# Kernel optimization log

Hardware: AMD Instinct MI355X
Metric: run time of the kernel (lower is better)

Reference implementation:

```python
import jax, jax.numpy as jnp
import numpy as np

N = 1_048_576   # nodes
E = 8_388_608   # edges
G = 32_768      # graphs
D = 9           # node embedding dim (hardcoded emb_dim=9 in source)
H = 2 * D       # GIN MLP hidden
L = 3           # num_layers
ATOM_V, BOND_V = 119, 6
BN_EPS = 1e-5


def setup_inputs() -> dict:
    key = jax.random.key(0)
    ks = jax.random.split(key, 12)
    f = lambda i, shape: jax.random.normal(ks[i], shape, jnp.float32) * 0.1
    return {
        'atom_emb': f(0, (9, ATOM_V, D)),
        'bond_emb': f(1, (L, 3, BOND_V, D)),
        'eps_gin': jnp.zeros((L,), jnp.float32),
        'W1': f(2, (L, D, H)), 'b1': jnp.zeros((L, H)),
        'bn1_g': jnp.ones((L, H)), 'bn1_b': jnp.zeros((L, H)),
        'W2': f(3, (L, H, D)), 'b2': jnp.zeros((L, D)),
        'bno_g': jnp.ones((L, D)), 'bno_b': jnp.zeros((L, D)),
        'vnW1': f(4, (L - 1, D, H)), 'vnb1': jnp.zeros((L - 1, H)),
        'vnbn1_g': jnp.ones((L - 1, H)), 'vnbn1_b': jnp.zeros((L - 1, H)),
        'vnW2': f(5, (L - 1, H, D)), 'vnb2': jnp.zeros((L - 1, D)),
        'vnbn2_g': jnp.ones((L - 1, D)), 'vnbn2_b': jnp.zeros((L - 1, D)),
        'x': jax.random.randint(ks[6], (N, 9), 0, 2),
        'edge_index': jax.random.randint(ks[7], (2, E), 0, N),
        'edge_attr': jax.random.randint(ks[8], (E, 3), 0, 2),
        'batch': jnp.sort(jax.random.randint(ks[9], (N,), 0, G)),
        'num_graphs': G,
    }


def _bn(h, g, b):
    # BatchNorm1d in training mode: batch mean / biased variance
    m = h.mean(axis=0)
    v = h.var(axis=0)
    return (h - m) * jax.lax.rsqrt(v + BN_EPS) * g + b


def reference(atom_emb, bond_emb, eps_gin, W1, b1, bn1_g, bn1_b, W2, b2,
              bno_g, bno_b, vnW1, vnb1, vnbn1_g, vnbn1_b, vnW2, vnb2,
              vnbn2_g, vnbn2_b, x, edge_index, edge_attr, batch, num_graphs):
    n_nodes = x.shape[0]
    src, dst = edge_index[0], edge_index[1]
    # AtomEncoder: sum of per-field embeddings -> [N, D]
    h = atom_emb[jnp.arange(atom_emb.shape[0])[None, :], x].sum(axis=1)
    vn = jnp.zeros((num_graphs, h.shape[1]), h.dtype)  # virtualnode emb init 0
    num_layers = W1.shape[0]
    for l in range(num_layers):
        h_in = h + vn[batch]                              # broadcast VN to nodes
        # BondEncoder for this layer -> [E, D]
        e = bond_emb[l][jnp.arange(3)[None, :], edge_attr].sum(axis=1)
        # GIN message: relu(x_j + e), sum-aggregate at target
        msg = jax.nn.relu(h_in[src] + e)
        aggr = jax.ops.segment_sum(msg, dst, num_segments=n_nodes)
        z = (1.0 + eps_gin[l]) * h_in + aggr
        z = jax.nn.relu(_bn(z @ W1[l] + b1[l], bn1_g[l], bn1_b[l])) @ W2[l] + b2[l]
        z = _bn(z, bno_g[l], bno_b[l])
        if l < num_layers - 1:
            z = jax.nn.relu(z)
        h_new = z + h_in                                   # residual=True
        if l < num_layers - 1:
            vn_tmp = jax.ops.segment_sum(h_in, batch, num_segments=num_graphs) + vn
            t = jax.nn.relu(_bn(vn_tmp @ vnW1[l] + vnb1[l], vnbn1_g[l], vnbn1_b[l]))
            t = jax.nn.relu(_bn(t @ vnW2[l] + vnb2[l], vnbn2_g[l], vnbn2_b[l]))
            vn = vn + t                                    # VN residual
        h = h_new
    pooled = jax.ops.segment_sum(h, batch, num_segments=num_graphs)  # global_add_pool
    return jnp.sum(pooled, axis=0, keepdims=True)          # [1, D]
```

## Files before the change

### kernel.cpp

```cpp
#include <hip/hip_runtime.h>
#include <hip/hip_fp8.h>

#define NN 1048576
#define NE 8388608
#define NG 32768
#define DD 9
#define SB 12
#define HH 18
#define BN_EPS 1e-5f

#define NPB 512
#define NB  2048
#define NGRP 64
#define P1B 512
#define P3MAX 5120
#define P3KEYS 4096

#define NSUM1 0
#define NSQ1  18
#define NSUM2 36
#define NSQ2  45
#define OUTS  54
#define VBASE 4096
#define VSUM1 (VBASE+0)
#define VSQ1  (VBASE+18)
#define VSUM2 (VBASE+36)
#define VSQ2  (VBASE+45)
#define STATS_FLOATS 4224

typedef float fv4 __attribute__((ext_vector_type(4)));

__device__ __forceinline__ float waveReduce(float v) {
#pragma unroll
  for (int off = 32; off > 0; off >>= 1) v += __shfl_down(v, off, 64);
  return v;
}
__device__ __forceinline__ unsigned f8enc(float f) {
  __hip_fp8_e4m3 v(f);
  return (unsigned)v.__x;
}
__device__ __forceinline__ float f8dec(unsigned b) {
  __hip_fp8_e4m3 v;
  v.__x = (__hip_fp8_storage_t)b;
  return (float)v;
}


__global__ void __launch_bounds__(1024)
k_counthist(const int* __restrict__ ei, int* __restrict__ cnt_pad,
            int* __restrict__ blkcnt) {
  __shared__ int hist[NB];
  int tid = threadIdx.x;
  for (int i = tid; i < NB; i += 1024) hist[i] = 0;
  __syncthreads();
  const int CH = NE / P1B;
  int base = blockIdx.x * CH;
  for (int i = tid; i < CH; i += 1024)
    atomicAdd(&hist[ei[NE + base + i] >> 9], 1);
  __syncthreads();
  for (int i = tid; i < NB; i += 1024)
    if (hist[i]) atomicAdd(&cnt_pad[i * 16], hist[i]);
  if (tid < NGRP) {
    int s = 0;
#pragma unroll
    for (int k = 0; k < 32; ++k) s += hist[tid * 32 + k];
    blkcnt[tid * P1B + blockIdx.x] = s;
  }
}

__global__ void k_scan(const int* __restrict__ cnt_pad, int* __restrict__ bucket_base,
                       int* __restrict__ bucket_cursor) {
  __shared__ int tsum[256];
  int tid = threadIdx.x;
  int c[8];
  int run = 0;
#pragma unroll
  for (int k = 0; k < 8; ++k) { c[k] = cnt_pad[(tid * 8 + k) * 16]; run += c[k]; }
  tsum[tid] = run;
  __syncthreads();
  for (int off = 1; off < 256; off <<= 1) {
    int v = (tid >= off) ? tsum[tid - off] : 0;
    __syncthreads();
    tsum[tid] += v;
    __syncthreads();
  }
  int excl = tsum[tid] - run;
#pragma unroll
  for (int k = 0; k < 8; ++k) {
    bucket_base[tid * 8 + k] = excl;
    bucket_cursor[tid * 8 + k] = excl;
    excl += c[k];
  }
  if (tid == 255) bucket_base[NB] = tsum[255];
}

__global__ void k_scanG(int* __restrict__ blkcnt, const int* __restrict__ bucket_base) {
  __shared__ int tsum[256];
  int tid = threadIdx.x;
  int g = blockIdx.x;
  int c0 = blkcnt[g * P1B + 2 * tid], c1 = blkcnt[g * P1B + 2 * tid + 1];
  int run = c0 + c1;
  tsum[tid] = run;
  __syncthreads();
  for (int off = 1; off < 256; off <<= 1) {
    int v = (tid >= off) ? tsum[tid - off] : 0;
    __syncthreads();
    tsum[tid] += v;
    __syncthreads();
  }
  int excl = tsum[tid] - run + bucket_base[g << 5];
  blkcnt[g * P1B + 2 * tid] = excl;
  blkcnt[g * P1B + 2 * tid + 1] = excl + c0;
}

__global__ void __launch_bounds__(1024)
k_p1(const int* __restrict__ ei, const int* __restrict__ ea,
     const int* __restrict__ blkcnt, uint2* __restrict__ coarse) {
  __shared__ int lcnt[NGRP];
  __shared__ int lbase[NGRP];
  int tid = threadIdx.x;
  if (tid < NGRP) { lcnt[tid] = 0; lbase[tid] = blkcnt[tid * P1B + blockIdx.x]; }
  __syncthreads();
  const int CH = NE / P1B;
  int base = blockIdx.x * CH;
  for (int k = 0; k < CH / 1024; ++k) {
    int e = base + k * 1024 + tid;
    int s = ei[e];
    int d = ei[NE + e];
    unsigned at = (unsigned)((ea[(size_t)e * 3 + 0] & 1) |
                             ((ea[(size_t)e * 3 + 1] & 1) << 1) |
                             ((ea[(size_t)e * 3 + 2] & 1) << 2));
    int g = d >> 14;
    int pos = atomicAdd(&lcnt[g], 1);
    coarse[lbase[g] + pos] = make_uint2((unsigned)s | (at << 20), (unsigned)d);
  }
}

#define P2K 48
#define P2SUB 32
__global__ void __launch_bounds__(256)
k_p2(const uint2* __restrict__ coarse, const int* __restrict__ bucket_base,
     int* __restrict__ bucket_cursor, unsigned* __restrict__ binned) {
  __shared__ unsigned stage[32 * P2K];
  __shared__ int scnt[32], gbase[32];
  int tid = threadIdx.x;
  int g = blockIdx.x >> 5;
  int sub = blockIdx.x & 31;
  int s0 = bucket_base[g << 5];
  int s1 = bucket_base[(g + 1) << 5];
  int len = s1 - s0;
  int chunk = (len + P2SUB - 1) >> 5;
  int my0 = s0 + sub * chunk;
  int my1 = min(my0 + chunk, s1);
  if (tid < 32) scnt[tid] = 0;
  __syncthreads();
  for (int b0 = my0; b0 < my1; b0 += 1024) {
#pragma unroll
    for (int k = 0; k < 4; ++k) {
      int i = b0 + k * 256 + tid;
      if (i < my1) {
        uint2 rec = coarse[i];
        unsigned s = rec.x & 0xFFFFFu;
        unsigned at = rec.x >> 20;
        unsigned d = rec.y;
        int bt = (int)((d >> 9) & 31u);
        unsigned o = s | ((d & 511u) << 20) | (at << 29);
        int pos = atomicAdd(&scnt[bt], 1);
        if (pos < P2K) stage[bt * P2K + pos] = o;
        else binned[atomicAdd(&bucket_cursor[(g << 5) | bt], 1)] = o;
      }
    }
    __syncthreads();
    {
      int bt = tid >> 3, j = tid & 7;
      int cnt = min(scnt[bt], P2K);
      if (j == 0) gbase[bt] = cnt ? atomicAdd(&bucket_cursor[(g << 5) | bt], cnt) : 0;
      __syncthreads();
      for (int i = j; i < cnt; i += 8) binned[gbase[bt] + i] = stage[bt * P2K + i];
    }
    __syncthreads();
    if (tid < 32) scnt[tid] = 0;
    __syncthreads();
  }
}

__global__ void __launch_bounds__(256)
k_p3(unsigned* __restrict__ binned, const int* __restrict__ bucket_base,
     int* __restrict__ row_ptr) {
  __shared__ int cnt[P3KEYS];
  __shared__ int tsum[256];
  __shared__ unsigned stage[P3MAX];
  int tid = threadIdx.x;
  int b = blockIdx.x;
  int s0 = bucket_base[b], s1 = bucket_base[b + 1];
  int len = s1 - s0;
  for (int i = tid; i < P3KEYS; i += 256) cnt[i] = 0;
  __syncthreads();
  for (int i = tid; i < len; i += 256) {
    unsigned rec = binned[s0 + i];
    int key = (int)((((rec >> 20) & 511u) << 3) | ((rec & 0xFFFFFu) >> 17));
    atomicAdd(&cnt[key], 1);
  }
  __syncthreads();
  int c[16];
  int run = 0;
#pragma unroll
  for (int k = 0; k < 16; ++k) { c[k] = cnt[tid * 16 + k]; run += c[k]; }
  tsum[tid] = run;
  __syncthreads();
  for (int off = 1; off < 256; off <<= 1) {
    int v = (tid >= off) ? tsum[tid - off] : 0;
    __syncthreads();
    tsum[tid] += v;
    __syncthreads();
  }
  int excl = tsum[tid] - run;
  int sum8 = 0;
#pragma unroll
  for (int k = 0; k < 8; ++k) sum8 += c[k];
  row_ptr[b * NPB + 2 * tid] = s0 + excl;
  row_ptr[b * NPB + 2 * tid + 1] = s0 + excl + sum8;
  if (b == NB - 1 && tid == 255) row_ptr[NN] = s0 + excl + run;
  int e = excl;
#pragma unroll
  for (int k = 0; k < 16; ++k) { cnt[tid * 16 + k] = e; e += c[k]; }
  __syncthreads();
  for (int i = tid; i < len; i += 256) {
    unsigned rec = binned[s0 + i];
    int key = (int)((((rec >> 20) & 511u) << 3) | ((rec & 0xFFFFFu) >> 17));
    int pos = atomicAdd(&cnt[key], 1);
    stage[pos] = (rec & 0xFFFFFu) | ((rec >> 29) << 20);
  }
  __syncthreads();
  for (int i = tid; i < len; i += 256) binned[s0 + i] = stage[i];
}


__device__ __forceinline__ void writeMirror(uint2* __restrict__ hmA,
                                            unsigned char* __restrict__ hmB,
                                            size_t n, const float* hv) {
  uint2 q;
  q.x = f8enc(hv[0]) | (f8enc(hv[1]) << 8) | (f8enc(hv[2]) << 16) | (f8enc(hv[3]) << 24);
  q.y = f8enc(hv[4]) | (f8enc(hv[5]) << 8) | (f8enc(hv[6]) << 16) | (f8enc(hv[7]) << 24);
  hmA[n] = q;
  hmB[n] = (unsigned char)f8enc(hv[8]);
}

__global__ void k_atom(const float* __restrict__ atom_emb, const int* __restrict__ x,
                       const int* __restrict__ batch, float* __restrict__ h,
                       uint2* __restrict__ hmA, unsigned char* __restrict__ hmB,
                       float* __restrict__ vnsum) {
  int n = blockIdx.x * 256 + threadIdx.x;
  int xi[9];
#pragma unroll
  for (int f = 0; f < 9; ++f) xi[f] = x[(size_t)n * 9 + f];
  float acc[DD] = {0.f,0.f,0.f,0.f,0.f,0.f,0.f,0.f,0.f};
#pragma unroll
  for (int f = 0; f < 9; ++f) {
    const float* row = atom_emb + ((size_t)f * 119 + xi[f]) * DD;
#pragma unroll
    for (int d = 0; d < DD; ++d) acc[d] += row[d];
  }
  float* o = h + (size_t)n * SB;
  ((float4*)o)[0] = make_float4(acc[0], acc[1], acc[2], acc[3]);
  ((float4*)o)[1] = make_float4(acc[4], acc[5], acc[6], acc[7]);
  o[8] = acc[8];
  writeMirror(hmA, hmB, (size_t)n, acc);
  int g = batch[n];
  int lane = threadIdx.x & 63;
  float s[DD];
#pragma unroll
  for (int d = 0; d < DD; ++d) s[d] = acc[d];
#pragma unroll
  for (int st = 1; st < 64; st <<= 1) {
    int gu = __shfl_up(g, st, 64);
    bool ok = (lane >= st) && (gu == g);
#pragma unroll
    for (int d = 0; d < DD; ++d) {
      float vu = __shfl_up(s[d], st, 64);
      if (ok) s[d] += vu;
    }
  }
  int gn = __shfl_down(g, 1, 64);
  if ((lane == 63) || (gn != g)) {
#pragma unroll
    for (int d = 0; d < DD; ++d) atomicAdd(&vnsum[(size_t)g * DD + d], s[d]);
  }
}

__device__ __forceinline__ void edgeDecodeAcc(unsigned r, uint2 q, unsigned db,
                                              const float* __restrict__ comb,
                                              float* __restrict__ acc) {
  const float* cb = comb + (r >> 20) * DD;
  float hv[DD] = {f8dec(q.x & 255u), f8dec((q.x >> 8) & 255u),
                  f8dec((q.x >> 16) & 255u), f8dec(q.x >> 24),
                  f8dec(q.y & 255u), f8dec((q.y >> 8) & 255u),
                  f8dec((q.y >> 16) & 255u), f8dec(q.y >> 24),
                  f8dec(db)};
#pragma unroll
  for (int d = 0; d < DD; ++d) {
    float m = hv[d] + cb[d];
    m = m > 0.f ? m : 0.f;
    acc[d] += m;
  }
}

__device__ __forceinline__ void accumNode(const unsigned* __restrict__ binned,
                                          int e0, int e1,
                                          const uint2* __restrict__ hmA,
                                          const unsigned char* __restrict__ hmB,
                                          const float* __restrict__ comb,
                                          float* __restrict__ acc) {
  int i = e0;
  for (; i + 4 <= e1; i += 4) {
    unsigned r0 = binned[i], r1 = binned[i + 1], r2 = binned[i + 2], r3 = binned[i + 3];
    uint2 q0 = hmA[r0 & 0xFFFFFu];
    uint2 q1 = hmA[r1 & 0xFFFFFu];
    uint2 q2 = hmA[r2 & 0xFFFFFu];
    uint2 q3 = hmA[r3 & 0xFFFFFu];
    unsigned char d0 = hmB[r0 & 0xFFFFFu];
    unsigned char d1 = hmB[r1 & 0xFFFFFu];
    unsigned char d2 = hmB[r2 & 0xFFFFFu];
    unsigned char d3 = hmB[r3 & 0xFFFFFu];
    edgeDecodeAcc(r0, q0, d0, comb, acc);
    edgeDecodeAcc(r1, q1, d1, comb, acc);
    edgeDecodeAcc(r2, q2, d2, comb, acc);
    edgeDecodeAcc(r3, q3, d3, comb, acc);
  }
  for (; i < e1; ++i) {
    unsigned r = binned[i];
    uint2 q = hmA[r & 0xFFFFFu];
    unsigned char db = hmB[r & 0xFFFFFu];
    edgeDecodeAcc(r, q, db, comb, acc);
  }
}

__global__ void __launch_bounds__(256, 8)
k_edgeA(const float* __restrict__ hbuf, const uint2* __restrict__ hmA,
        const unsigned char* __restrict__ hmB, const unsigned* __restrict__ binned,
        const int* __restrict__ row_ptr, const float* __restrict__ bond,
        const float* __restrict__ W1l, const float* __restrict__ b1l,
        const float* __restrict__ epsp, float* __restrict__ X,
        float* __restrict__ stats) {
  __shared__ float comb[8 * DD];
  __shared__ float sW1[DD * HH], sb1[HH], ssum[HH], ssq[HH];
  int tid = threadIdx.x;
  for (int i = tid; i < DD * HH; i += 256) sW1[i] = W1l[i];
  if (tid < 8 * DD) {
    int c = tid / DD, d = tid % DD;
    comb[tid] = bond[(0 * 6 + (c & 1)) * DD + d] +
                bond[(1 * 6 + ((c >> 1) & 1)) * DD + d] +
                bond[(2 * 6 + ((c >> 2) & 1)) * DD + d];
  }
  if (tid < HH) { sb1[tid] = b1l[tid]; ssum[tid] = 0.f; ssq[tid] = 0.f; }
  __syncthreads();

  int b = blockIdx.x;
  int nA = b * NPB + tid;
  int nB = nA + 256;
  int ea0 = row_ptr[nA], ea1 = row_ptr[nA + 1];
  int eb0 = row_ptr[nB], eb1 = row_ptr[nB + 1];
  float acc0[DD] = {0.f,0.f,0.f,0.f,0.f,0.f,0.f,0.f,0.f};
  float acc1[DD] = {0.f,0.f,0.f,0.f,0.f,0.f,0.f,0.f,0.f};
  accumNode(binned, ea0, ea1, hmA, hmB, comb, acc0);
  accumNode(binned, eb0, eb1, hmA, hmB, comb, acc1);

  float eps1 = 1.0f + epsp[0];
  float z0[DD], z1[DD];
  {
    const float* hr = hbuf + (size_t)nA * SB;
    float4 HA = ((const float4*)hr)[0], HB = ((const float4*)hr)[1];
    float h8 = hr[8];
    float hi[DD] = {HA.x, HA.y, HA.z, HA.w, HB.x, HB.y, HB.z, HB.w, h8};
#pragma unroll
    for (int d = 0; d < DD; ++d) z0[d] = eps1 * hi[d] + acc0[d];
    float* xo = X + (size_t)nA * SB;
    fv4 v0 = {z0[0], z0[1], z0[2], z0[3]};
    fv4 v1 = {z0[4], z0[5], z0[6], z0[7]};
    __builtin_nontemporal_store(v0, (fv4*)xo);
    __builtin_nontemporal_store(v1, (fv4*)(xo + 4));
    __builtin_nontemporal_store(z0[8], xo + 8);
  }
  {
    const float* hr = hbuf + (size_t)nB * SB;
    float4 HA = ((const float4*)hr)[0], HB = ((const float4*)hr)[1];
    float h8 = hr[8];
    float hi[DD] = {HA.x, HA.y, HA.z, HA.w, HB.x, HB.y, HB.z, HB.w, h8};
#pragma unroll
    for (int d = 0; d < DD; ++d) z1[d] = eps1 * hi[d] + acc1[d];
    float* xo = X + (size_t)nB * SB;
    fv4 v0 = {z1[0], z1[1], z1[2], z1[3]};
    fv4 v1 = {z1[4], z1[5], z1[6], z1[7]};
    __builtin_nontemporal_store(v0, (fv4*)xo);
    __builtin_nontemporal_store(v1, (fv4*)(xo + 4));
    __builtin_nontemporal_store(z1[8], xo + 8);
  }
  int lane0 = ((tid & 63) == 0);
#pragma unroll
  for (int j = 0; j < HH; ++j) {
    float a0 = sb1[j], a1 = sb1[j];
#pragma unroll
    for (int d = 0; d < DD; ++d) {
      a0 += z0[d] * sW1[d * HH + j];
      a1 += z1[d] * sW1[d * HH + j];
    }
    float rs = waveReduce(a0 + a1);
    float rq = waveReduce(a0 * a0 + a1 * a1);
    if (lane0) { atomicAdd(&ssum[j], rs); atomicAdd(&ssq[j], rq); }
  }
  __syncthreads();
  int copy = (b & 63) * 64;
  if (tid < HH) {
    atomicAdd(&stats[copy + NSUM1 + tid], ssum[tid]);
    atomicAdd(&stats[copy + NSQ1 + tid], ssq[tid]);
  }
}

__global__ void __launch_bounds__(256)
k_partB(float* __restrict__ X, const float* __restrict__ W1l, const float* __restrict__ b1l,
        const float* __restrict__ g1, const float* __restrict__ be1,
        const float* __restrict__ W2l, const float* __restrict__ b2l,
        float* __restrict__ stats) {
  __shared__ float sW1[DD * HH], sW2[HH * DD], sb1[HH], sb2[DD];
  __shared__ float sc1[HH], sh1[HH], ssum[DD], ssq[DD];
  int tid = threadIdx.x;
  for (int i = tid; i < DD * HH; i += 256) sW1[i] = W1l[i];
  for (int i = tid; i < HH * DD; i += 256) sW2[i] = W2l[i];
  if (tid < HH) {
    float s = 0.f, q = 0.f;
#pragma unroll
    for (int c = 0; c < 64; ++c) {
      s += stats[c * 64 + NSUM1 + tid];
      q += stats[c * 64 + NSQ1 + tid];
    }
    float mean = s * (1.0f / NN);
    float var = q * (1.0f / NN) - mean * mean;
    float sc = g1[tid] * rsqrtf(var + BN_EPS);
    sc1[tid] = sc;
    sh1[tid] = be1[tid] - mean * sc;
    sb1[tid] = b1l[tid];
  }
  if (tid < DD) { sb2[tid] = b2l[tid]; ssum[tid] = 0.f; ssq[tid] = 0.f; }
  __syncthreads();
  size_t n = (size_t)blockIdx.x * 256 + tid;
  float* xr = X + n * SB;
  fv4 XA = __builtin_nontemporal_load((const fv4*)xr);
  fv4 XB = __builtin_nontemporal_load((const fv4*)(xr + 4));
  float x8 = __builtin_nontemporal_load(xr + 8);
  float z[DD] = {XA.x, XA.y, XA.z, XA.w, XB.x, XB.y, XB.z, XB.w, x8};
  float t[HH];
#pragma unroll
  for (int j = 0; j < HH; ++j) {
    float a = sb1[j];
#pragma unroll
    for (int d = 0; d < DD; ++d) a += z[d] * sW1[d * HH + j];
    a = a * sc1[j] + sh1[j];
    t[j] = a > 0.f ? a : 0.f;
  }
  float z2[DD];
  int lane0 = ((tid & 63) == 0);
#pragma unroll
  for (int d = 0; d < DD; ++d) {
    float a = sb2[d];
#pragma unroll
    for (int j = 0; j < HH; ++j) a += t[j] * sW2[j * DD + d];
    z2[d] = a;
    float rs = waveReduce(a);
    float rq = waveReduce(a * a);
    if (lane0) { atomicAdd(&ssum[d], rs); atomicAdd(&ssq[d], rq); }
  }
  fv4 v0 = {z2[0], z2[1], z2[2], z2[3]};
  fv4 v1 = {z2[4], z2[5], z2[6], z2[7]};
  __builtin_nontemporal_store(v0, (fv4*)xr);
  __builtin_nontemporal_store(v1, (fv4*)(xr + 4));
  __builtin_nontemporal_store(z2[8], xr + 8);
  __syncthreads();
  int copy = ((int)blockIdx.x & 63) * 64;
  if (tid < DD) {
    atomicAdd(&stats[copy + NSUM2 + tid], ssum[tid]);
    atomicAdd(&stats[copy + NSQ2 + tid], ssq[tid]);
  }
}

__global__ void __launch_bounds__(256)
k_partC(const float* __restrict__ X, float* __restrict__ hbuf,
        uint2* __restrict__ hmA, unsigned char* __restrict__ hmB,
        float* __restrict__ stats, const float* __restrict__ g2,
        const float* __restrict__ be2, const int* __restrict__ batch,
        const float* __restrict__ vn_next, float* __restrict__ vnsum_out,
        int do_relu) {
  __shared__ float sc[DD], sh[DD], ssum[DD];
  int tid = threadIdx.x;
  if (tid < DD) {
    float s = 0.f, q = 0.f;
#pragma unroll
    for (int c = 0; c < 64; ++c) {
      s += stats[c * 64 + NSUM2 + tid];
      q += stats[c * 64 + NSQ2 + tid];
    }
    float mean = s * (1.0f / NN);
    float var = q * (1.0f / NN) - mean * mean;
    float sg = g2[tid] * rsqrtf(var + BN_EPS);
    sc[tid] = sg;
    sh[tid] = be2[tid] - mean * sg;
    ssum[tid] = 0.f;
  }
  __syncthreads();
  size_t n = (size_t)blockIdx.x * 256 + tid;
  const float* xr = X + n * SB;
  fv4 XA = __builtin_nontemporal_load((const fv4*)xr);
  fv4 XB = __builtin_nontemporal_load((const fv4*)(xr + 4));
  float x8 = __builtin_nontemporal_load(xr + 8);
  float zv[DD] = {XA.x, XA.y, XA.z, XA.w, XB.x, XB.y, XB.z, XB.w, x8};
  float* hr = hbuf + n * SB;
  float4 HA = ((float4*)hr)[0], HB = ((float4*)hr)[1];
  float h8 = hr[8];
  float hi[DD] = {HA.x, HA.y, HA.z, HA.w, HB.x, HB.y, HB.z, HB.w, h8};
  float hv[DD];
#pragma unroll
  for (int d = 0; d < DD; ++d) {
    float z = zv[d] * sc[d] + sh[d];
    if (do_relu) z = z > 0.f ? z : 0.f;
    hv[d] = z + hi[d];
  }
  if (vn_next != nullptr) {
    int g = batch[n];
#pragma unroll
    for (int d = 0; d < DD; ++d) hv[d] += vn_next[(size_t)g * DD + d];
    ((float4*)hr)[0] = make_float4(hv[0], hv[1], hv[2], hv[3]);
    ((float4*)hr)[1] = make_float4(hv[4], hv[5], hv[6], hv[7]);
    hr[8] = hv[8];
    writeMirror(hmA, hmB, n, hv);
    if (vnsum_out != nullptr) {
      int lane = tid & 63;
      float s[DD];
#pragma unroll
      for (int d = 0; d < DD; ++d) s[d] = hv[d];
#pragma unroll
      for (int st = 1; st < 64; st <<= 1) {
        int gu = __shfl_up(g, st, 64);
        bool ok = (lane >= st) && (gu == g);
#pragma unroll
        for (int d = 0; d < DD; ++d) {
          float vu = __shfl_up(s[d], st, 64);
          if (ok) s[d] += vu;
        }
      }
      int gn = __shfl_down(g, 1, 64);
      if ((lane == 63) || (gn != g)) {
#pragma unroll
        for (int d = 0; d < DD; ++d) atomicAdd(&vnsum_out[(size_t)g * DD + d], s[d]);
      }
    }
  } else {
    int lane0 = ((tid & 63) == 0);
#pragma unroll
    for (int d = 0; d < DD; ++d) {
      float r = waveReduce(hv[d]);
      if (lane0) atomicAdd(&ssum[d], r);
    }
    __syncthreads();
    int copy = ((int)blockIdx.x & 63) * 64;
    if (tid < DD) atomicAdd(&stats[copy + OUTS + tid], ssum[tid]);
  }
}

__global__ void k_out(const float* __restrict__ stats, float* __restrict__ out) {
  int tid = threadIdx.x;
  if (tid < DD) {
    float s = 0.f;
#pragma unroll
    for (int c = 0; c < 64; ++c) s += stats[c * 64 + OUTS + tid];
    out[tid] = s;
  }
}


__global__ void k_vnA(const float* __restrict__ vnsum, const float* __restrict__ vn,
                      float* __restrict__ vt1, const float* __restrict__ W1l,
                      const float* __restrict__ b1l, float* __restrict__ stats) {
  __shared__ float sW[DD * HH], sb[HH], ssum[HH], ssq[HH];
  int tid = threadIdx.x;
  for (int i = tid; i < DD * HH; i += 256) sW[i] = W1l[i];
  if (tid < HH) { sb[tid] = b1l[tid]; ssum[tid] = 0.f; ssq[tid] = 0.f; }
  __syncthreads();
  size_t g = (size_t)blockIdx.x * 256 + tid;
  float r[DD];
#pragma unroll
  for (int d = 0; d < DD; ++d) r[d] = vnsum[g * DD + d] + vn[g * DD + d];
  int lane0 = ((tid & 63) == 0);
#pragma unroll
  for (int j = 0; j < HH; ++j) {
    float a = sb[j];
#pragma unroll
    for (int d = 0; d < DD; ++d) a += r[d] * sW[d * HH + j];
    vt1[g * HH + j] = a;
    float rs = waveReduce(a);
    float rq = waveReduce(a * a);
    if (lane0) { atomicAdd(&ssum[j], rs); atomicAdd(&ssq[j], rq); }
  }
  __syncthreads();
  if (tid < HH) {
    atomicAdd(&stats[VSUM1 + tid], ssum[tid]);
    atomicAdd(&stats[VSQ1 + tid], ssq[tid]);
  }
}

__global__ void k_vnB(const float* __restrict__ vt1, float* __restrict__ vt2,
                      const float* __restrict__ W2l, const float* __restrict__ b2l,
                      const float* __restrict__ g1, const float* __restrict__ be1,
                      float* __restrict__ stats) {
  __shared__ float sW2[HH * DD], sb2[DD], sc1[HH], sh1[HH], ssum[DD], ssq[DD];
  int tid = threadIdx.x;
  for (int i = tid; i < HH * DD; i += 256) sW2[i] = W2l[i];
  if (tid < HH) {
    float mean = stats[VSUM1 + tid] * (1.0f / NG);
    float var = stats[VSQ1 + tid] * (1.0f / NG) - mean * mean;
    float sc = g1[tid] * rsqrtf(var + BN_EPS);
    sc1[tid] = sc;
    sh1[tid] = be1[tid] - mean * sc;
  }
  if (tid < DD) { sb2[tid] = b2l[tid]; ssum[tid] = 0.f; ssq[tid] = 0.f; }
  __syncthreads();
  size_t g = (size_t)blockIdx.x * 256 + tid;
  float t[HH];
#pragma unroll
  for (int j = 0; j < HH; ++j) {
    float a = vt1[g * HH + j] * sc1[j] + sh1[j];
    t[j] = a > 0.f ? a : 0.f;
  }
  int lane0 = ((tid & 63) == 0);
#pragma unroll
  for (int d = 0; d < DD; ++d) {
    float a = sb2[d];
#pragma unroll
    for (int j = 0; j < HH; ++j) a += t[j] * sW2[j * DD + d];
    vt2[g * DD + d] = a;
    float rs = waveReduce(a);
    float rq = waveReduce(a * a);
    if (lane0) { atomicAdd(&ssum[d], rs); atomicAdd(&ssq[d], rq); }
  }
  __syncthreads();
  if (tid < DD) {
    atomicAdd(&stats[VSUM2 + tid], ssum[tid]);
    atomicAdd(&stats[VSQ2 + tid], ssq[tid]);
  }
}

__global__ void k_vnC(const float* __restrict__ vt2, float* __restrict__ vn,
                      const float* __restrict__ g2, const float* __restrict__ be2,
                      const float* __restrict__ stats) {
  __shared__ float sc[DD], sh[DD];
  int tid = threadIdx.x;
  if (tid < DD) {
    float mean = stats[VSUM2 + tid] * (1.0f / NG);
    float var = stats[VSQ2 + tid] * (1.0f / NG) - mean * mean;
    float s = g2[tid] * rsqrtf(var + BN_EPS);
    sc[tid] = s;
    sh[tid] = be2[tid] - mean * s;
  }
  __syncthreads();
  size_t g = (size_t)blockIdx.x * 256 + tid;
#pragma unroll
  for (int d = 0; d < DD; ++d) {
    float v = vt2[g * DD + d] * sc[d] + sh[d];
    v = v > 0.f ? v : 0.f;
    vn[g * DD + d] += v;
  }
}

extern "C" void kernel_launch(void* const* d_in, const int* in_sizes, int n_in,
                              void* d_out, int out_size, void* d_ws, size_t ws_size,
                              hipStream_t stream) {
  const float* atom_emb = (const float*)d_in[0];
  const float* bond_emb = (const float*)d_in[1];
  const float* eps_gin  = (const float*)d_in[2];
  const float* W1   = (const float*)d_in[3];
  const float* b1   = (const float*)d_in[4];
  const float* bn1_g = (const float*)d_in[5];
  const float* bn1_b = (const float*)d_in[6];
  const float* W2   = (const float*)d_in[7];
  const float* b2   = (const float*)d_in[8];
  const float* bno_g = (const float*)d_in[9];
  const float* bno_b = (const float*)d_in[10];
  const float* vnW1 = (const float*)d_in[11];
  const float* vnb1 = (const float*)d_in[12];
  const float* vnbn1_g = (const float*)d_in[13];
  const float* vnbn1_b = (const float*)d_in[14];
  const float* vnW2 = (const float*)d_in[15];
  const float* vnb2 = (const float*)d_in[16];
  const float* vnbn2_g = (const float*)d_in[17];
  const float* vnbn2_b = (const float*)d_in[18];
  const int* x          = (const int*)d_in[19];
  const int* edge_index = (const int*)d_in[20];
  const int* edge_attr  = (const int*)d_in[21];
  const int* batch      = (const int*)d_in[22];
  float* out = (float*)d_out;

  float* hbuf  = (float*)d_ws;
  float* X     = hbuf + (size_t)NN * SB;
  uint2* hmA   = (uint2*)(X + (size_t)NN * SB);
  unsigned char* hmB = (unsigned char*)(hmA + (size_t)NN);
  unsigned* binned = (unsigned*)(hmB + (size_t)NN);
  float* vn    = (float*)(binned + (size_t)NE);
  float* vnsum = vn + (size_t)NG * DD;
  float* vt2   = vnsum;
  float* vt1   = vnsum + (size_t)NG * DD;
  float* stats = vt1 + (size_t)NG * HH;
  int* bucket_base   = (int*)(stats + STATS_FLOATS);
  int* bucket_cursor = bucket_base + NB + 1;
  int* row_ptr       = bucket_cursor + NB;
  uint2* coarse = (uint2*)d_ws;
  int* cnt_pad  = (int*)((char*)d_ws + (size_t)NE * sizeof(uint2));
  int* blkcnt   = cnt_pad + (size_t)NB * 16;

  (void)hipMemsetAsync(cnt_pad, 0, (size_t)NB * 16 * sizeof(int), stream);
  k_counthist<<<P1B, 1024, 0, stream>>>(edge_index, cnt_pad, blkcnt);
  k_scan<<<1, 256, 0, stream>>>(cnt_pad, bucket_base, bucket_cursor);
  k_scanG<<<NGRP, 256, 0, stream>>>(blkcnt, bucket_base);
  k_p1<<<P1B, 1024, 0, stream>>>(edge_index, edge_attr, blkcnt, coarse);
  k_p2<<<NGRP * P2SUB, 256, 0, stream>>>(coarse, bucket_base, bucket_cursor, binned);
  k_p3<<<NB, 256, 0, stream>>>(binned, bucket_base, row_ptr);

  (void)hipMemsetAsync(vn, 0, (size_t)2 * NG * DD * sizeof(float), stream);
  k_atom<<<NN / 256, 256, 0, stream>>>(atom_emb, x, batch, hbuf, hmA, hmB, vnsum);

  for (int l = 0; l < 3; ++l) {
    int has_vn = (l < 2);
    (void)hipMemsetAsync(stats, 0, STATS_FLOATS * sizeof(float), stream);
    if (has_vn) {
      k_vnA<<<NG / 256, 256, 0, stream>>>(vnsum, vn, vt1, vnW1 + (size_t)l * DD * HH,
                                          vnb1 + (size_t)l * HH, stats);
      k_vnB<<<NG / 256, 256, 0, stream>>>(vt1, vt2, vnW2 + (size_t)l * HH * DD,
                                          vnb2 + (size_t)l * DD,
                                          vnbn1_g + (size_t)l * HH, vnbn1_b + (size_t)l * HH,
                                          stats);
      k_vnC<<<NG / 256, 256, 0, stream>>>(vt2, vn, vnbn2_g + (size_t)l * DD,
                                          vnbn2_b + (size_t)l * DD, stats);
    }
    k_edgeA<<<NB, 256, 0, stream>>>(hbuf, hmA, hmB, binned, row_ptr,
                                    bond_emb + (size_t)l * 3 * 6 * DD,
                                    W1 + (size_t)l * DD * HH, b1 + (size_t)l * HH,
                                    eps_gin + l, X, stats);
    k_partB<<<NN / 256, 256, 0, stream>>>(X, W1 + (size_t)l * DD * HH,
                                          b1 + (size_t)l * HH,
                                          bn1_g + (size_t)l * HH, bn1_b + (size_t)l * HH,
                                          W2 + (size_t)l * HH * DD, b2 + (size_t)l * DD,
                                          stats);
    if (l == 0)
      (void)hipMemsetAsync(vnsum, 0, (size_t)NG * DD * sizeof(float), stream);
    k_partC<<<NN / 256, 256, 0, stream>>>(X, hbuf, hmA, hmB, stats,
                                          bno_g + (size_t)l * DD, bno_b + (size_t)l * DD,
                                          batch,
                                          has_vn ? vn : nullptr,
                                          (l == 0) ? vnsum : nullptr,
                                          has_vn ? 1 : 0);
  }
  k_out<<<1, 64, 0, stream>>>(stats, out);
}
```

Measured before the change: 1.335 ms.

## Split per-node edge lists by source quarter and sync blocks between phases

The in-bucket sort key now uses source bits 18-19 (four source-address quarters) instead of three bits. For each node the kernel stores packed 8-bit offsets of the quarter boundaries in a new rpo array. k_edgeA walks each node's edges in four phases, one per source quarter, with a __syncthreads between phases. The aim is to keep all waves of a block gathering from the same region of the fp8 node mirror at the same time, for better cache locality. The cost is extra barriers and an extra per-node array, and the 8-bit offsets assume no node has more than 255 edges.

```diff
diff --git a/kernel.cpp b/kernel.cpp
--- a/kernel.cpp
+++ b/kernel.cpp
@@ -14,7 +14,7 @@
 #define NGRP 64
 #define P1B 512
 #define P3MAX 5120
-#define P3KEYS 4096
+#define P3KEYS 2048
 
 #define NSUM1 0
 #define NSQ1  18
@@ -186,7 +186,7 @@
 
 __global__ void __launch_bounds__(256)
 k_p3(unsigned* __restrict__ binned, const int* __restrict__ bucket_base,
-     int* __restrict__ row_ptr) {
+     int* __restrict__ row_ptr, unsigned* __restrict__ rpo) {
   __shared__ int cnt[P3KEYS];
   __shared__ int tsum[256];
   __shared__ unsigned stage[P3MAX];
@@ -198,14 +198,14 @@
   __syncthreads();
   for (int i = tid; i < len; i += 256) {
     unsigned rec = binned[s0 + i];
-    int key = (int)((((rec >> 20) & 511u) << 3) | ((rec & 0xFFFFFu) >> 17));
+    int key = (int)((((rec >> 20) & 511u) << 2) | ((rec & 0xFFFFFu) >> 18));
     atomicAdd(&cnt[key], 1);
   }
   __syncthreads();
-  int c[16];
+  int c[8];
   int run = 0;
 #pragma unroll
-  for (int k = 0; k < 16; ++k) { c[k] = cnt[tid * 16 + k]; run += c[k]; }
+  for (int k = 0; k < 8; ++k) { c[k] = cnt[tid * 8 + k]; run += c[k]; }
   tsum[tid] = run;
   __syncthreads();
   for (int off = 1; off < 256; off <<= 1) {
@@ -215,19 +215,28 @@
     __syncthreads();
   }
   int excl = tsum[tid] - run;
-  int sum8 = 0;
-#pragma unroll
-  for (int k = 0; k < 8; ++k) sum8 += c[k];
+  int sum4 = c[0] + c[1] + c[2] + c[3];
   row_ptr[b * NPB + 2 * tid] = s0 + excl;
-  row_ptr[b * NPB + 2 * tid + 1] = s0 + excl + sum8;
+  row_ptr[b * NPB + 2 * tid + 1] = s0 + excl + sum4;
   if (b == NB - 1 && tid == 255) row_ptr[NN] = s0 + excl + run;
+  {
+    unsigned roA = 0, roB = 0;
+    int rA = 0, rB = 0;
+#pragma unroll
+    for (int k = 0; k < 4; ++k) {
+      rA += c[k];      roA |= (unsigned)rA << (k * 8);
+      rB += c[4 + k];  roB |= (unsigned)rB << (k * 8);
+    }
+    rpo[(size_t)b * NPB + 2 * tid] = roA;
+    rpo[(size_t)b * NPB + 2 * tid + 1] = roB;
+  }
   int e = excl;
 #pragma unroll
-  for (int k = 0; k < 16; ++k) { cnt[tid * 16 + k] = e; e += c[k]; }
+  for (int k = 0; k < 8; ++k) { cnt[tid * 8 + k] = e; e += c[k]; }
   __syncthreads();
   for (int i = tid; i < len; i += 256) {
     unsigned rec = binned[s0 + i];
-    int key = (int)((((rec >> 20) & 511u) << 3) | ((rec & 0xFFFFFu) >> 17));
+    int key = (int)((((rec >> 20) & 511u) << 2) | ((rec & 0xFFFFFu) >> 18));
     int pos = atomicAdd(&cnt[key], 1);
     stage[pos] = (rec & 0xFFFFFu) | ((rec >> 29) << 20);
   }
@@ -338,7 +347,8 @@
 __global__ void __launch_bounds__(256, 8)
 k_edgeA(const float* __restrict__ hbuf, const uint2* __restrict__ hmA,
         const unsigned char* __restrict__ hmB, const unsigned* __restrict__ binned,
-        const int* __restrict__ row_ptr, const float* __restrict__ bond,
+        const int* __restrict__ row_ptr, const unsigned* __restrict__ rpo,
+        const float* __restrict__ bond,
         const float* __restrict__ W1l, const float* __restrict__ b1l,
         const float* __restrict__ epsp, float* __restrict__ X,
         float* __restrict__ stats) {
@@ -358,12 +368,23 @@
   int b = blockIdx.x;
   int nA = b * NPB + tid;
   int nB = nA + 256;
-  int ea0 = row_ptr[nA], ea1 = row_ptr[nA + 1];
-  int eb0 = row_ptr[nB], eb1 = row_ptr[nB + 1];
+  int ea0 = row_ptr[nA];
+  int eb0 = row_ptr[nB];
+  unsigned roA = rpo[nA], roB = rpo[nB];
   float acc0[DD] = {0.f,0.f,0.f,0.f,0.f,0.f,0.f,0.f,0.f};
   float acc1[DD] = {0.f,0.f,0.f,0.f,0.f,0.f,0.f,0.f,0.f};
-  accumNode(binned, ea0, ea1, hmA, hmB, comb, acc0);
-  accumNode(binned, eb0, eb1, hmA, hmB, comb, acc1);
+
+  int pA = ea0, pB = eb0;
+#pragma unroll
+  for (int q = 0; q < 4; ++q) {
+    int eA = ea0 + (int)((roA >> (q * 8)) & 255u);
+    int eB = eb0 + (int)((roB >> (q * 8)) & 255u);
+    accumNode(binned, pA, eA, hmA, hmB, comb, acc0);
+    accumNode(binned, pB, eB, hmA, hmB, comb, acc1);
+    pA = eA;
+    pB = eB;
+    __syncthreads();
+  }
 
   float eps1 = 1.0f + epsp[0];
   float z0[DD], z1[DD];
@@ -710,6 +731,7 @@
   int* bucket_base   = (int*)(stats + STATS_FLOATS);
   int* bucket_cursor = bucket_base + NB + 1;
   int* row_ptr       = bucket_cursor + NB;
+  unsigned* rpo      = (unsigned*)(row_ptr + NN + 1);
   uint2* coarse = (uint2*)d_ws;
   int* cnt_pad  = (int*)((char*)d_ws + (size_t)NE * sizeof(uint2));
   int* blkcnt   = cnt_pad + (size_t)NB * 16;
@@ -720,7 +742,7 @@
   k_scanG<<<NGRP, 256, 0, stream>>>(blkcnt, bucket_base);
   k_p1<<<P1B, 1024, 0, stream>>>(edge_index, edge_attr, blkcnt, coarse);
   k_p2<<<NGRP * P2SUB, 256, 0, stream>>>(coarse, bucket_base, bucket_cursor, binned);
-  k_p3<<<NB, 256, 0, stream>>>(binned, bucket_base, row_ptr);
+  k_p3<<<NB, 256, 0, stream>>>(binned, bucket_base, row_ptr, rpo);
 
   (void)hipMemsetAsync(vn, 0, (size_t)2 * NG * DD * sizeof(float), stream);
   k_atom<<<NN / 256, 256, 0, stream>>>(atom_emb, x, batch, hbuf, hmA, hmB, vnsum);
@@ -738,7 +760,7 @@
       k_vnC<<<NG / 256, 256, 0, stream>>>(vt2, vn, vnbn2_g + (size_t)l * DD,
                                           vnbn2_b + (size_t)l * DD, stats);
     }
-    k_edgeA<<<NB, 256, 0, stream>>>(hbuf, hmA, hmB, binned, row_ptr,
+    k_edgeA<<<NB, 256, 0, stream>>>(hbuf, hmA, hmB, binned, row_ptr, rpo,
                                     bond_emb + (size_t)l * 3 * 6 * DD,
                                     W1 + (size_t)l * DD * HH, b1 + (size_t)l * HH,
                                     eps_gin + l, X, stats);
```

Measured after the change: 1.330 ms. Within noise of the previous version (-0.4%).
